# Kernel tuning notes

Hardware: AMD Instinct MI355X
Metric: run time of the kernel (lower is better)

## Reference

```python
import jax, jax.numpy as jnp
import numpy as np

D_MODEL = 192
D_INNER = 384          # expand(2) * d_model
HEADDIM = 12
NHEADS = 32            # d_inner // headdim
DSTATE = 16
NGROUPS = 1
CONV_DIM = D_INNER + 2 * NGROUPS * DSTATE          # 416
D_IN_PROJ = 2 * D_INNER + 2 * NGROUPS * DSTATE + NHEADS  # 832
LN_EPS = 1e-5


def silu(x):
    return x * jax.nn.sigmoid(x)


def depthwise_conv2d(x_nchw, w, b):
    # groups == channels depthwise conv, kernel 3, padding 1 (SAME)
    out = jax.lax.conv_general_dilated(
        x_nchw, w, window_strides=(1, 1), padding='SAME',
        feature_group_count=CONV_DIM,
        dimension_numbers=('NCHW', 'OIHW', 'NCHW'))
    return out + b[None, :, None, None]


def setup_inputs() -> dict:
    key = jax.random.key(0)
    ks = jax.random.split(key, 10)
    Bn, H, W = 4, 128, 128
    u = jax.random.normal(ks[0], (Bn, H, W, D_MODEL), jnp.float32)
    t = jax.random.normal(ks[1], (Bn, H, W, D_MODEL), jnp.float32)
    s_in = 1.0 / np.sqrt(D_MODEL)
    W_in = jax.random.normal(ks[2], (D_IN_PROJ, D_MODEL), jnp.float32) * s_in
    W_t_in = jax.random.normal(ks[3], (D_IN_PROJ, D_MODEL), jnp.float32) * s_in
    conv_w = jax.random.normal(ks[4], (CONV_DIM, 1, 3, 3), jnp.float32) * (1.0 / 3.0)
    conv_b = jnp.zeros((CONV_DIM,), jnp.float32)
    # dt_bias = inverse-softplus of dt sampled log-uniform in [dt_min, dt_max]
    dt0 = jnp.exp(jax.random.uniform(ks[5], (NHEADS,)) * (np.log(0.1) - np.log(0.001)) + np.log(0.001))
    dt_bias = dt0 + jnp.log(-jnp.expm1(-dt0))
    A_log = jnp.log(jax.random.uniform(ks[6], (NHEADS,), minval=1.0, maxval=16.0))
    D = jnp.ones((NHEADS,), jnp.float32)
    ln_gamma = jnp.ones((D_INNER,), jnp.float32)
    ln_beta = jnp.zeros((D_INNER,), jnp.float32)
    W_out = jax.random.normal(ks[7], (D_MODEL, D_INNER), jnp.float32) * (1.0 / np.sqrt(D_INNER))
    return dict(u=u, t=t, W_in=W_in, W_t_in=W_t_in, conv_w=conv_w, conv_b=conv_b,
                dt_bias=dt_bias, A_log=A_log, D=D, ln_gamma=ln_gamma, ln_beta=ln_beta,
                W_out=W_out)


def reference(u, t, W_in, W_t_in, conv_w, conv_b, dt_bias, A_log, D,
              ln_gamma, ln_beta, W_out):
    B0, H, W_, C0 = u.shape
    L = H * W_
    uu = u.reshape(B0, L, C0)
    tt = t.reshape(B0, L, C0)

    # in_proj on main branch: split into z, xBC, dt
    zxbcdt = uu @ W_in.T                                    # (B, L, 832)
    z = zxbcdt[..., :D_INNER]                               # (B, L, 384)
    xBC = zxbcdt[..., D_INNER:D_INNER + CONV_DIM]           # (B, L, 416)
    dt = zxbcdt[..., D_INNER + CONV_DIM:]                   # (B, L, 32)
    dt = jax.nn.softplus(dt + dt_bias)

    # t branch: only x1B1C1 part is ultimately used (C := C1)
    x1B1C1 = (tt @ W_t_in.T)[..., D_INNER:D_INNER + CONV_DIM]

    # depthwise 3x3 conv + silu on both branches
    xBC = xBC.reshape(B0, H, W_, CONV_DIM).transpose(0, 3, 1, 2)
    xBC = silu(depthwise_conv2d(xBC, conv_w, conv_b))
    xBC = xBC.transpose(0, 2, 3, 1).reshape(B0, L, CONV_DIM)

    x1B1C1 = x1B1C1.reshape(B0, H, W_, CONV_DIM).transpose(0, 3, 1, 2)
    x1B1C1 = silu(depthwise_conv2d(x1B1C1, conv_w, conv_b))
    x1B1C1 = x1B1C1.transpose(0, 2, 3, 1).reshape(B0, L, CONV_DIM)

    x = xBC[..., :D_INNER]                                  # V features (B, L, 384)
    Bk = xBC[..., D_INNER:D_INNER + NGROUPS * DSTATE]       # K (B, L, 16)
    Cq = x1B1C1[..., D_INNER + NGROUPS * DSTATE:]           # Q from t-branch (B, L, 16)

    A = -jnp.exp(A_log)                                     # (nheads,), negative

    # non-causal linear attention duality (ngroups == 1)
    V = x.reshape(B0, L, NHEADS, HEADDIM).transpose(0, 2, 1, 3)   # (B, h, L, d)
    dtT = dt.transpose(0, 2, 1)                                   # (B, h, L)
    dA = -(dtT[..., None] * A[None, :, None, None])               # ssd_positve_dA: positive
    V_scaled = V * dA
    KV = jnp.einsum('bln,bhld->bhnd', Bk, V_scaled)               # (B, h, 16, 12)
    y = jnp.einsum('bln,bhnd->bhld', Cq, KV) + V * D[None, :, None, None]
    y = y.transpose(0, 2, 1, 3).reshape(B0, L, D_INNER)

    # LayerNorm over d_inner
    mu = jnp.mean(y, axis=-1, keepdims=True)
    var = jnp.mean((y - mu) ** 2, axis=-1, keepdims=True)
    y = (y - mu) * jax.lax.rsqrt(var + LN_EPS) * ln_gamma + ln_beta

    y = y * z
    out = y @ W_out.T
    return out.reshape(B0, H, W_, C0)
```

## Files before the change

kernel.cpp:

```cpp
#include <hip/hip_runtime.h>
#include <hip/hip_bf16.h>
#include <math.h>


#define BN 4
#define HH 128
#define WWID 128
#define LTOK (HH*WWID)
#define NTOK (BN*LTOK)
#define DMODEL 192
#define DINNER 384
#define NH 32
#define HD 12
#define DST 16
#define CONVD 416
#define KVCHUNKS 64
#define PM 256
#define TILE_SH 12288
#define TILE_BY 24576
#define TROW ((size_t)NTOK*64)
#define YPAD 392

typedef __hip_bfloat16 bf16;
typedef unsigned int uint32;
typedef unsigned short ushort16;
typedef __attribute__((ext_vector_type(8))) short bf16x8;
typedef __attribute__((ext_vector_type(4))) float f32x4;
typedef __attribute__((ext_vector_type(16))) float f32x16;

__device__ __forceinline__ float bflo(uint32 v){ return __uint_as_float((v & 0xffffu) << 16); }
__device__ __forceinline__ float bfhi(uint32 v){ return __uint_as_float(v & 0xffff0000u); }
__device__ __forceinline__ ushort16 f2bf(float f){
    __hip_bfloat16 h = __float2bfloat16(f);
    return *reinterpret_cast<const ushort16*>(&h);
}
__device__ __forceinline__ float ldbf(const bf16* p){
    return __uint_as_float(((uint32)(*(const ushort16*)p)) << 16);
}
__device__ __forceinline__ float ldbfs(const short* p){
    return __uint_as_float(((uint32)(ushort16)(*p)) << 16);
}
__device__ __forceinline__ float softplusf(float x){
    return (x > 20.f) ? x : log1pf(expf(x));
}
__device__ __forceinline__ float siluf(float x){
    return x / (1.f + expf(-x));
}

union BFPK { short s[8]; bf16x8 v; };

__global__ __launch_bounds__(256) void k_prep(
    const float* __restrict__ Win, const float* __restrict__ Wout,
    const float* __restrict__ cw,
    bf16* __restrict__ Wsw, bf16* __restrict__ Wout_sh, float* __restrict__ wtr)
{
    const int i = blockIdx.x*256 + threadIdx.x;
    if (i < 832*DMODEL) {
        const int ch = i / DMODEL, k = i - ch*DMODEL;
        const int nt = ch >> 6, row = ch & 63;
        const int ks = k ^ ((row & 7) << 3);
        Wsw[(size_t)nt*TILE_SH + row*DMODEL + ks] = __float2bfloat16(Win[i]);
    }
    if (i < DMODEL*DINNER) {
        const int m = i / DINNER, k = i - m*DINNER;
        const int ni = m >> 4, mr = m & 15;
        const int ks = k >> 5, kq = (k >> 3) & 3, ii = k & 7;
        const int lane = kq*16 + mr;
        Wout_sh[(size_t)((ni*12 + ks)*64 + lane)*8 + ii] = __float2bfloat16(Wout[i]);
    }
    if (i < CONVD*9) { const int c = i/9, k = i - c*9; wtr[k*420 + c] = cw[i]; }
}

__global__ __launch_bounds__(512) void k_proj_mfma(
    const float* __restrict__ u, const bf16* __restrict__ Wsw,
    const float* __restrict__ dt_b, const float* __restrict__ A_log,
    bf16* __restrict__ z_bf, bf16* __restrict__ xbc_pre, float* __restrict__ dA)
{
    __shared__ __align__(16) short S[3*TILE_SH];

    const int tid = threadIdx.x;
    const int m0 = blockIdx.x * PM;
    const int ntbase = blockIdx.y * 7;
    const int ntiles = blockIdx.y ? 6 : 7;
    const int wid = tid >> 6, lane = tid & 63;
    const int fr = lane & 31;
    const int hi = lane >> 5;

    const char* gW = (const char*)Wsw;
    auto GLOAD = [&](int nt, int buf) {
        const char* src = gW + (size_t)nt*TILE_BY + wid*3072 + lane*16;
        char* dst = ((char*)S) + buf*TILE_BY + wid*3072;
        #pragma unroll
        for (int c = 0; c < 3; ++c)
            __builtin_amdgcn_global_load_lds(
                (const __attribute__((address_space(1))) void*)(src + c*1024),
                (__attribute__((address_space(3))) void*)(dst + c*1024), 16, 0, 0);
    };

    GLOAD(ntbase, 0);

    const float db = dt_b[fr];
    const float al = expf(A_log[fr]);
    bf16x8 a[12];
    {
        const float* arow = u + (size_t)(m0 + wid*32 + fr)*DMODEL;
        #pragma unroll
        for (int ks=0;ks<12;++ks) {
            const float4 a0 = *(const float4*)(arow + ks*16 + hi*8);
            const float4 a1 = *(const float4*)(arow + ks*16 + hi*8 + 4);
            BFPK pk;
            pk.s[0]=(short)f2bf(a0.x); pk.s[1]=(short)f2bf(a0.y);
            pk.s[2]=(short)f2bf(a0.z); pk.s[3]=(short)f2bf(a0.w);
            pk.s[4]=(short)f2bf(a1.x); pk.s[5]=(short)f2bf(a1.y);
            pk.s[6]=(short)f2bf(a1.z); pk.s[7]=(short)f2bf(a1.w);
            a[ks] = pk.v;
        }
    }
    asm volatile("s_waitcnt vmcnt(0)" ::: "memory");
    GLOAD(ntbase + 1, 1);
    __builtin_amdgcn_s_barrier();
    __builtin_amdgcn_sched_barrier(0);

    const int kswz = (fr & 7) << 3;

    for (int i = 0; i < ntiles; ++i) {
        const int nt = ntbase + i;
        const short* Sb = &S[(i % 3)*TILE_SH];

        f32x16 acc0, acc1;
        #pragma unroll
        for (int q=0;q<16;++q) { acc0[q]=0.f; acc1[q]=0.f; }

        #pragma unroll
        for (int ks=0;ks<12;++ks) {
            const int kk = (ks*16 + hi*8) ^ kswz;
            const bf16x8 b0 = *(const bf16x8*)&Sb[fr*DMODEL + kk];
            const bf16x8 b1 = *(const bf16x8*)&Sb[(32+fr)*DMODEL + kk];
            acc0 = __builtin_amdgcn_mfma_f32_32x32x16_bf16(a[ks], b0, acc0, 0, 0, 0);
            acc1 = __builtin_amdgcn_mfma_f32_32x32x16_bf16(a[ks], b1, acc1, 0, 0, 0);
        }

        #pragma unroll
        for (int ni=0;ni<2;++ni) {
            const f32x16& ac = ni ? acc1 : acc0;
            const int n0 = nt*64 + ni*32;
            if (n0 < DINNER) {
                bf16* dst = z_bf + (size_t)nt*TROW + (ni*32 + fr);
                #pragma unroll
                for (int r=0;r<16;++r) {
                    const int tok = m0 + wid*32 + (r&3) + 8*(r>>2) + 4*hi;
                    dst[(size_t)tok*64] = __float2bfloat16(ac[r]);
                }
            } else if (n0 < 800) {
                const int loc = n0 - DINNER + fr;
                bf16* dst = xbc_pre + (size_t)(loc>>6)*TROW + (loc & 63);
                #pragma unroll
                for (int r=0;r<16;++r) {
                    const int tok = m0 + wid*32 + (r&3) + 8*(r>>2) + 4*hi;
                    dst[(size_t)tok*64] = __float2bfloat16(ac[r]);
                }
            } else {
                #pragma unroll
                for (int r=0;r<16;++r) {
                    const int tok = m0 + wid*32 + (r&3) + 8*(r>>2) + 4*hi;
                    const float dt = softplusf(ac[r] + db);
                    dA[(size_t)tok*NH + fr] = dt * al;
                }
            }
        }

        if (i + 2 < ntiles) {
            GLOAD(nt + 2, (i + 2) % 3);
            asm volatile("s_waitcnt vmcnt(35)" ::: "memory");
        } else {
            asm volatile("s_waitcnt vmcnt(32)" ::: "memory");
        }
        __builtin_amdgcn_s_barrier();
        __builtin_amdgcn_sched_barrier(0);
    }
}

__global__ __launch_bounds__(256) void k_tproj(
    const float* __restrict__ t, const float* __restrict__ Wtin, float* __restrict__ cq_pre)
{
    __shared__ float ts[16][196];
    __shared__ float ws[16][196];
    const int tid = threadIdx.x;
    const int tok0 = blockIdx.x * 16;
    #pragma unroll
    for (int i = 0; i < 3; ++i) {
        const int flat = tid + 256*i;
        const int row = flat / 48, c = (flat % 48)*4;
        *(float4*)&ts[row][c] = *(const float4*)(t    + (size_t)(tok0+row)*DMODEL + c);
        *(float4*)&ws[row][c] = *(const float4*)(Wtin + (size_t)(784+row)*DMODEL + c);
    }
    __syncthreads();
    const int tt = tid >> 4, n = tid & 15;
    float s0=0.f,s1=0.f,s2=0.f,s3=0.f;
    #pragma unroll 4
    for (int k = 0; k < DMODEL; k += 4) {
        s0 = fmaf(ts[tt][k+0], ws[n][k+0], s0);
        s1 = fmaf(ts[tt][k+1], ws[n][k+1], s1);
        s2 = fmaf(ts[tt][k+2], ws[n][k+2], s2);
        s3 = fmaf(ts[tt][k+3], ws[n][k+3], s3);
    }
    cq_pre[(size_t)(tok0+tt)*DST + n] = (s0+s1)+(s2+s3);
}

__global__ __launch_bounds__(416) void k_conv416(
    const bf16* __restrict__ in, const float* __restrict__ wtr, const float* __restrict__ cb,
    bf16* __restrict__ out)
{
    __shared__ float ws[9*420];
    __shared__ float bs[416];
    const int tid = threadIdx.x;
    for (int i = tid; i < 9*420; i += 416) ws[i] = wtr[i];
    if (tid < 416) bs[tid] = cb[tid];
    __syncthreads();

    const int pl  = tid / 52;
    const int grp = tid - pl*52;
    const int c0  = grp*8;
    const int pix = blockIdx.x*8 + pl;
    const int hw  = pix & (LTOK-1);
    const int h = hw >> 7, w = hw & 127;
    const int bb = pix >> 14;

    const bf16* inT = in + (size_t)(c0 >> 6)*TROW + (c0 & 63);

    float acc[8];
    {
        const float4 b0 = *(const float4*)&bs[c0];
        const float4 b1 = *(const float4*)&bs[c0+4];
        acc[0]=b0.x; acc[1]=b0.y; acc[2]=b0.z; acc[3]=b0.w;
        acc[4]=b1.x; acc[5]=b1.y; acc[6]=b1.z; acc[7]=b1.w;
    }

    #pragma unroll
    for (int dh=-1; dh<=1; ++dh) {
        const int hh = h + dh;
        if ((unsigned)hh >= (unsigned)HH) continue;
        #pragma unroll
        for (int dw=-1; dw<=1; ++dw) {
            const int w2 = w + dw;
            if ((unsigned)w2 >= (unsigned)WWID) continue;
            const int wi = (dh+1)*3 + (dw+1);
            const int pix2 = (bb<<14) + (hh<<7) + w2;
            const uint4 v = *(const uint4*)((const ushort16*)inT + (size_t)pix2*64);
            const float4 w0 = *(const float4*)&ws[wi*420 + c0];
            const float4 w1 = *(const float4*)&ws[wi*420 + c0 + 4];
            acc[0] = fmaf(bflo(v.x), w0.x, acc[0]);
            acc[1] = fmaf(bfhi(v.x), w0.y, acc[1]);
            acc[2] = fmaf(bflo(v.y), w0.z, acc[2]);
            acc[3] = fmaf(bfhi(v.y), w0.w, acc[3]);
            acc[4] = fmaf(bflo(v.z), w1.x, acc[4]);
            acc[5] = fmaf(bfhi(v.z), w1.y, acc[5]);
            acc[6] = fmaf(bflo(v.w), w1.z, acc[6]);
            acc[7] = fmaf(bfhi(v.w), w1.w, acc[7]);
        }
    }

    uint4 o;
    o.x = ((uint32)f2bf(siluf(acc[1])) << 16) | (uint32)f2bf(siluf(acc[0]));
    o.y = ((uint32)f2bf(siluf(acc[3])) << 16) | (uint32)f2bf(siluf(acc[2]));
    o.z = ((uint32)f2bf(siluf(acc[5])) << 16) | (uint32)f2bf(siluf(acc[4]));
    o.w = ((uint32)f2bf(siluf(acc[7])) << 16) | (uint32)f2bf(siluf(acc[6]));
    *(uint4*)((ushort16*)out + (size_t)pix*CONVD + c0) = o;
}

__global__ __launch_bounds__(256) void k_conv16(
    const float* __restrict__ in, const float* __restrict__ cw, const float* __restrict__ cb,
    bf16* __restrict__ out)
{
    const int idx = blockIdx.x*256 + threadIdx.x;
    const int cc = idx & 15;
    const int pix = idx >> 4;
    const int hw = pix & (LTOK-1);
    const int h = hw >> 7, w = hw & 127;
    const int bb = pix >> 14;
    const int c = 400 + cc;

    float wg[9];
    #pragma unroll
    for (int k=0;k<9;++k) wg[k] = cw[c*9+k];
    float a = cb[c];
    #pragma unroll
    for (int dh=-1; dh<=1; ++dh) {
        const int hh = h + dh;
        if ((unsigned)hh >= (unsigned)HH) continue;
        #pragma unroll
        for (int dw=-1; dw<=1; ++dw) {
            const int w2 = w + dw;
            if ((unsigned)w2 >= (unsigned)WWID) continue;
            a = fmaf(in[((size_t)((bb<<14)+(hh<<7)+w2))*16 + cc], wg[(dh+1)*3 + (dw+1)], a);
        }
    }
    out[(size_t)pix*16 + cc] = __float2bfloat16(siluf(a));
}

__global__ __launch_bounds__(512) void k_kv(
    const bf16* __restrict__ xbc_post, const float* __restrict__ dA,
    float* __restrict__ partial)
{
    __shared__ short vsb[16][408];
    __shared__ float das[16][32];
    const int tid = threadIdx.x;
    const int b = blockIdx.y;
    const int n = tid & 15;
    const int g = tid >> 4;

    float acc[12];
    #pragma unroll
    for (int j=0;j<12;++j) acc[j]=0.f;

    const int l0base = b*LTOK + blockIdx.x*256;

    for (int it = 0; it < 16; ++it) {
        const int l0 = l0base + it*16;
        for (int i = tid; i < 16*200; i += 512) {
            const int tok = i / 200;
            const int c2 = i - tok*200;
            const uint32 v = *(const uint32*)((const ushort16*)xbc_post
                                + (size_t)(l0+tok)*CONVD + c2*2);
            *(uint32*)&vsb[tok][c2*2] = v;
        }
        {
            const int tok = tid >> 5, h = tid & 31;
            das[tok][h] = dA[(size_t)(l0+tok)*NH + h];
        }
        __syncthreads();

        #pragma unroll
        for (int tok = 0; tok < 16; ++tok) {
            const uint32 bkraw = (uint32)(ushort16)vsb[tok][DINNER + n];
            const float s = __uint_as_float(bkraw << 16) * das[tok][g];
            const uint32* vp = (const uint32*)&vsb[tok][g*12];
            const uint32 w0 = vp[0], w1 = vp[1], w2 = vp[2];
            acc[0]  = fmaf(s, bflo(w0), acc[0]);
            acc[1]  = fmaf(s, bfhi(w0), acc[1]);
            acc[2]  = fmaf(s, bflo(w1), acc[2]);
            acc[3]  = fmaf(s, bfhi(w1), acc[3]);
            acc[4]  = fmaf(s, bflo(w2), acc[4]);
            acc[5]  = fmaf(s, bfhi(w2), acc[5]);
            const uint32* vq = (const uint32*)&vsb[tok][g*12 + 6];
            const uint32 w3 = vq[0], w4 = vq[1], w5 = vq[2];
            acc[6]  = fmaf(s, bflo(w3), acc[6]);
            acc[7]  = fmaf(s, bfhi(w3), acc[7]);
            acc[8]  = fmaf(s, bflo(w4), acc[8]);
            acc[9]  = fmaf(s, bfhi(w4), acc[9]);
            acc[10] = fmaf(s, bflo(w5), acc[10]);
            acc[11] = fmaf(s, bfhi(w5), acc[11]);
        }
        __syncthreads();
    }

    float* dst = partial + ((size_t)(b*KVCHUNKS + blockIdx.x))*6144 + (size_t)tid*12;
    #pragma unroll
    for (int j4=0;j4<3;++j4)
        *(float4*)(dst + j4*4) = make_float4(acc[j4*4], acc[j4*4+1], acc[j4*4+2], acc[j4*4+3]);
}

__global__ __launch_bounds__(256) void k_kvred(
    const float* __restrict__ partial, bf16* __restrict__ kvhl)
{
    const int idx = blockIdx.x*256 + threadIdx.x;
    const int b = idx / 6144;
    const int rem = idx - b*6144;
    const int hd = rem >> 4, n = rem & 15;
    const int h = hd / HD, d = hd - h*HD;
    const float* p = partial + (size_t)(b*KVCHUNKS)*6144 + h*192 + n*12 + d;
    float s = 0.f;
    #pragma unroll 4
    for (int c = 0; c < KVCHUNKS; ++c) s += p[(size_t)c*6144];
    const bf16 hi = __float2bfloat16(s);
    const float hif = ldbf(&hi);
    kvhl[((size_t)b*2 + 0)*6144 + rem] = hi;
    kvhl[((size_t)b*2 + 1)*6144 + rem] = __float2bfloat16(s - hif);
}

__global__ __launch_bounds__(256) void k_ynorm_out(
    const bf16* __restrict__ xbc_post, const bf16* __restrict__ cq_bf,
    const bf16* __restrict__ z_bf, const bf16* __restrict__ kvhl,
    const float* __restrict__ Dv, const float* __restrict__ ln_g, const float* __restrict__ ln_b,
    const bf16* __restrict__ Wout_sh, float* __restrict__ out)
{
    __shared__ __align__(16) short yzs[64*YPAD];
    __shared__ float gs[DINNER], bs2[DINNER], ds[DINNER];
    const int tid = threadIdx.x;
    const int token0 = blockIdx.x * 64;
    const int b = token0 >> 14;

    {
        const int row = tid >> 2, seg = tid & 3;
        const short* src = (const short*)xbc_post + (size_t)(token0+row)*CONVD + seg*96;
        short* dst = &yzs[row*YPAD + seg*96];
        #pragma unroll
        for (int j = 0; j < 12; ++j)
            *(uint4*)(dst + j*8) = *(const uint4*)(src + j*8);
    }

    for (int i = tid; i < DINNER; i += 256) {
        gs[i]  = ln_g[i];
        bs2[i] = ln_b[i];
        ds[i]  = Dv[i/HD];
    }
    __syncthreads();

    const int wid = tid >> 6, lane = tid & 63;
    const int fr = lane & 15, fq = lane >> 4;
    const int tokA = token0 + wid*16;

    const bf16x8 cqf = *(const bf16x8*)((const short*)cq_bf + (size_t)(tokA+fr)*DST + (fq&1)*8);

    const short* kvsrc = (const short*)kvhl + ((size_t)b*2 + (fq >> 1))*6144
                         + (size_t)fr*16 + (fq & 1)*8;

    f32x4 acc[24];
    #pragma unroll
    for (int t = 0; t < 24; ++t) {
        const bf16x8 bfv = *(const bf16x8*)(kvsrc + t*256);
        f32x4 z4 = (f32x4){0.f,0.f,0.f,0.f};
        acc[t] = __builtin_amdgcn_mfma_f32_16x16x32_bf16(cqf, bfv, z4, 0, 0, 0);
    }

    const int rloc0 = wid*16 + fq*4;
    const int tokj0 = tokA + fq*4;
    float s[4]  = {0.f,0.f,0.f,0.f};
    float s2[4] = {0.f,0.f,0.f,0.f};
    #pragma unroll
    for (int t = 0; t < 24; ++t) {
        const int hd = t*16 + fr;
        const float dvh = ds[hd];
        #pragma unroll
        for (int j = 0; j < 4; ++j) {
            const float vv = ldbfs(&yzs[(rloc0+j)*YPAD + hd]);
            const float y = fmaf(vv, dvh, acc[t][j]);
            acc[t][j] = y;
            s[j] += y;
            s2[j] = fmaf(y, y, s2[j]);
        }
    }
    #pragma unroll
    for (int j = 0; j < 4; ++j) {
        #pragma unroll
        for (int off = 8; off > 0; off >>= 1) {
            s[j]  += __shfl_xor(s[j],  off, 16);
            s2[j] += __shfl_xor(s2[j], off, 16);
        }
    }
    float mu[4], rs[4];
    #pragma unroll
    for (int j = 0; j < 4; ++j) {
        mu[j] = s[j] * (1.f/384.f);
        const float var = s2[j]*(1.f/384.f) - mu[j]*mu[j];
        rs[j] = rsqrtf(var + 1e-5f);
    }

    #pragma unroll
    for (int t = 0; t < 24; ++t) {
        const int hd = t*16 + fr;
        const float g = gs[hd], be = bs2[hd];
        const bf16* zsrc = z_bf + (size_t)(hd>>6)*TROW + (hd & 63);
        #pragma unroll
        for (int j = 0; j < 4; ++j) {
            const int tok = tokj0 + j;
            const float yn = fmaf((acc[t][j] - mu[j])*rs[j], g, be);
            const float zv = ldbf(zsrc + (size_t)tok*64);
            yzs[(rloc0+j)*YPAD + hd] = (short)f2bf(yn*zv);
        }
    }

    const short* yrow = &yzs[(wid*16 + fr)*YPAD];
    bf16x8 af[12];
    #pragma unroll
    for (int ks = 0; ks < 12; ++ks)
        af[ks] = *(const bf16x8*)(yrow + ks*32 + fq*8);

    f32x4 oacc[12];
    #pragma unroll
    for (int ni = 0; ni < 12; ++ni) oacc[ni] = (f32x4){0.f,0.f,0.f,0.f};

    #pragma unroll
    for (int ks = 0; ks < 12; ++ks) {
        #pragma unroll
        for (int ni = 0; ni < 12; ++ni) {
            const bf16x8 bw = *(const bf16x8*)((const short*)Wout_sh
                                + (size_t)((ni*12 + ks)*64 + lane)*8);
            oacc[ni] = __builtin_amdgcn_mfma_f32_16x16x32_bf16(af[ks], bw, oacc[ni], 0, 0, 0);
        }
    }

    #pragma unroll
    for (int ni = 0; ni < 12; ++ni) {
        const int n = ni*16 + fr;
        #pragma unroll
        for (int r = 0; r < 4; ++r)
            out[(size_t)(tokj0 + r)*DMODEL + n] = oacc[ni][r];
    }
}

extern "C" void kernel_launch(void* const* d_in, const int* in_sizes, int n_in,
                              void* d_out, int out_size, void* d_ws, size_t ws_size,
                              hipStream_t stream)
{
    const float* u      = (const float*)d_in[0];
    const float* t      = (const float*)d_in[1];
    const float* Win    = (const float*)d_in[2];
    const float* Wtin   = (const float*)d_in[3];
    const float* conv_w = (const float*)d_in[4];
    const float* conv_b = (const float*)d_in[5];
    const float* dt_b   = (const float*)d_in[6];
    const float* A_log  = (const float*)d_in[7];
    const float* Dv     = (const float*)d_in[8];
    const float* ln_g   = (const float*)d_in[9];
    const float* ln_bt  = (const float*)d_in[10];
    const float* W_out  = (const float*)d_in[11];
    float* out = (float*)d_out;

    char* p = (char*)d_ws;
    bf16* z_bf     = (bf16*)p;  p += (size_t)6*TROW*2;
    bf16* xbc_pre  = (bf16*)p;  p += (size_t)7*TROW*2;
    bf16* xbc_post = (bf16*)p;  p += (size_t)NTOK*CONVD*2;
    float* cq_pre  = (float*)p; p += (size_t)NTOK*DST*4;
    bf16* cq_bf    = (bf16*)p;  p += (size_t)NTOK*DST*2;
    float* dA      = (float*)p; p += (size_t)NTOK*NH*4;
    bf16* kvhl     = (bf16*)p;  p += (size_t)BN*2*6144*2;
    bf16* Wsw      = (bf16*)p;  p += (size_t)832*DMODEL*2;
    bf16* Wout_sh  = (bf16*)p;  p += (size_t)DMODEL*DINNER*2;
    float* wtr     = (float*)p; p += (size_t)9*420*4;

    float* kv_part = (float*)xbc_pre;

    k_prep<<<624, 256, 0, stream>>>(Win, W_out, conv_w, Wsw, Wout_sh, wtr);
    k_proj_mfma<<<dim3(NTOK/PM, 2), 512, 0, stream>>>(u, Wsw, dt_b, A_log, z_bf, xbc_pre, dA);
    k_tproj<<<NTOK/16, 256, 0, stream>>>(t, Wtin, cq_pre);
    k_conv416<<<NTOK/8, 416, 0, stream>>>(xbc_pre, wtr, conv_b, xbc_post);
    k_conv16<<<NTOK*16/256, 256, 0, stream>>>(cq_pre, conv_w, conv_b, cq_bf);
    k_kv<<<dim3(KVCHUNKS, BN), 512, 0, stream>>>(xbc_post, dA, kv_part);
    k_kvred<<<BN*6144/256, 256, 0, stream>>>(kv_part, kvhl);
    k_ynorm_out<<<NTOK/64, 256, 0, stream>>>(xbc_post, cq_bf, z_bf, kvhl,
                                             Dv, ln_g, ln_bt, Wout_sh, out);
}
```

Measured before the change: 291.7 us.

## Register-tile depthwise conv to 2x4 outputs per thread for input reuse

Each thread in the 416-channel depthwise conv now computes a 2-row by 4-column patch of output pixels instead of one. Each input pixel loaded from global memory is reused across every output that needs it, so one thread reads 4x6 pixels rather than 9 per output. The grid shrinks eightfold, and each block covers 2 rows by 32 columns. In exchange, register use rises (64 accumulators per thread), and fewer blocks may limit occupancy and latency hiding.

```diff
diff --git a/kernel.cpp b/kernel.cpp
--- a/kernel.cpp
+++ b/kernel.cpp
@@ -221,51 +221,78 @@
     const int pl  = tid / 52;
     const int grp = tid - pl*52;
     const int c0  = grp*8;
-    const int pix = blockIdx.x*8 + pl;
-    const int hw  = pix & (LTOK-1);
-    const int h = hw >> 7, w = hw & 127;
-    const int bb = pix >> 14;
+    const int bid = blockIdx.x;
+    const int bb  = bid >> 8;
+    const int rem = bid & 255;
+    const int h0  = (rem >> 2) << 1;
+    const int w0  = ((rem & 3) << 5) + pl*4;
 
     const bf16* inT = in + (size_t)(c0 >> 6)*TROW + (c0 & 63);
 
-    float acc[8];
+    float acc[2][4][8];
     {
         const float4 b0 = *(const float4*)&bs[c0];
         const float4 b1 = *(const float4*)&bs[c0+4];
-        acc[0]=b0.x; acc[1]=b0.y; acc[2]=b0.z; acc[3]=b0.w;
-        acc[4]=b1.x; acc[5]=b1.y; acc[6]=b1.z; acc[7]=b1.w;
-    }
-
-    #pragma unroll
-    for (int dh=-1; dh<=1; ++dh) {
-        const int hh = h + dh;
-        if ((unsigned)hh >= (unsigned)HH) continue;
-        #pragma unroll
-        for (int dw=-1; dw<=1; ++dw) {
-            const int w2 = w + dw;
-            if ((unsigned)w2 >= (unsigned)WWID) continue;
-            const int wi = (dh+1)*3 + (dw+1);
-            const int pix2 = (bb<<14) + (hh<<7) + w2;
-            const uint4 v = *(const uint4*)((const ushort16*)inT + (size_t)pix2*64);
-            const float4 w0 = *(const float4*)&ws[wi*420 + c0];
-            const float4 w1 = *(const float4*)&ws[wi*420 + c0 + 4];
-            acc[0] = fmaf(bflo(v.x), w0.x, acc[0]);
-            acc[1] = fmaf(bfhi(v.x), w0.y, acc[1]);
-            acc[2] = fmaf(bflo(v.y), w0.z, acc[2]);
-            acc[3] = fmaf(bfhi(v.y), w0.w, acc[3]);
-            acc[4] = fmaf(bflo(v.z), w1.x, acc[4]);
-            acc[5] = fmaf(bfhi(v.z), w1.y, acc[5]);
-            acc[6] = fmaf(bflo(v.w), w1.z, acc[6]);
-            acc[7] = fmaf(bfhi(v.w), w1.w, acc[7]);
-        }
-    }
-
-    uint4 o;
-    o.x = ((uint32)f2bf(siluf(acc[1])) << 16) | (uint32)f2bf(siluf(acc[0]));
-    o.y = ((uint32)f2bf(siluf(acc[3])) << 16) | (uint32)f2bf(siluf(acc[2]));
-    o.z = ((uint32)f2bf(siluf(acc[5])) << 16) | (uint32)f2bf(siluf(acc[4]));
-    o.w = ((uint32)f2bf(siluf(acc[7])) << 16) | (uint32)f2bf(siluf(acc[6]));
-    *(uint4*)((ushort16*)out + (size_t)pix*CONVD + c0) = o;
+        #pragma unroll
+        for (int v2 = 0; v2 < 2; ++v2)
+            #pragma unroll
+            for (int u = 0; u < 4; ++u) {
+                acc[v2][u][0]=b0.x; acc[v2][u][1]=b0.y;
+                acc[v2][u][2]=b0.z; acc[v2][u][3]=b0.w;
+                acc[v2][u][4]=b1.x; acc[v2][u][5]=b1.y;
+                acc[v2][u][6]=b1.z; acc[v2][u][7]=b1.w;
+            }
+    }
+
+    #pragma unroll
+    for (int dr=-1; dr<=2; ++dr) {
+        const int rr = h0 + dr;
+        if ((unsigned)rr >= (unsigned)HH) continue;
+        const int rowb = (bb<<14) + (rr<<7);
+        #pragma unroll
+        for (int dc=-1; dc<=4; ++dc) {
+            const int wc = w0 + dc;
+            if ((unsigned)wc >= (unsigned)WWID) continue;
+            const uint4 v = *(const uint4*)((const ushort16*)inT + (size_t)(rowb + wc)*64);
+            const float x0=bflo(v.x), x1=bfhi(v.x), x2=bflo(v.y), x3=bfhi(v.y);
+            const float x4=bflo(v.z), x5=bfhi(v.z), x6=bflo(v.w), x7=bfhi(v.w);
+            #pragma unroll
+            for (int v2 = 0; v2 < 2; ++v2) {
+                const int dh = dr - v2;
+                if (dh < -1 || dh > 1) continue;
+                #pragma unroll
+                for (int u = 0; u < 4; ++u) {
+                    const int dw = dc - u;
+                    if (dw < -1 || dw > 1) continue;
+                    const int wi = (dh+1)*3 + (dw+1);
+                    const float4 w0v = *(const float4*)&ws[wi*420 + c0];
+                    const float4 w1v = *(const float4*)&ws[wi*420 + c0 + 4];
+                    acc[v2][u][0]=fmaf(x0,w0v.x,acc[v2][u][0]);
+                    acc[v2][u][1]=fmaf(x1,w0v.y,acc[v2][u][1]);
+                    acc[v2][u][2]=fmaf(x2,w0v.z,acc[v2][u][2]);
+                    acc[v2][u][3]=fmaf(x3,w0v.w,acc[v2][u][3]);
+                    acc[v2][u][4]=fmaf(x4,w1v.x,acc[v2][u][4]);
+                    acc[v2][u][5]=fmaf(x5,w1v.y,acc[v2][u][5]);
+                    acc[v2][u][6]=fmaf(x6,w1v.z,acc[v2][u][6]);
+                    acc[v2][u][7]=fmaf(x7,w1v.w,acc[v2][u][7]);
+                }
+            }
+        }
+    }
+
+    const int pix00 = (bb<<14) + (h0<<7) + w0;
+    #pragma unroll
+    for (int v2 = 0; v2 < 2; ++v2) {
+        #pragma unroll
+        for (int u = 0; u < 4; ++u) {
+            uint4 o;
+            o.x = ((uint32)f2bf(siluf(acc[v2][u][1])) << 16) | (uint32)f2bf(siluf(acc[v2][u][0]));
+            o.y = ((uint32)f2bf(siluf(acc[v2][u][3])) << 16) | (uint32)f2bf(siluf(acc[v2][u][2]));
+            o.z = ((uint32)f2bf(siluf(acc[v2][u][5])) << 16) | (uint32)f2bf(siluf(acc[v2][u][4]));
+            o.w = ((uint32)f2bf(siluf(acc[v2][u][7])) << 16) | (uint32)f2bf(siluf(acc[v2][u][6]));
+            *(uint4*)((ushort16*)out + (size_t)(pix00 + v2*WWID + u)*CONVD + c0) = o;
+        }
+    }
 }
 
 __global__ __launch_bounds__(256) void k_conv16(
@@ -534,7 +561,7 @@
     k_prep<<<624, 256, 0, stream>>>(Win, W_out, conv_w, Wsw, Wout_sh, wtr);
     k_proj_mfma<<<dim3(NTOK/PM, 2), 512, 0, stream>>>(u, Wsw, dt_b, A_log, z_bf, xbc_pre, dA);
     k_tproj<<<NTOK/16, 256, 0, stream>>>(t, Wtin, cq_pre);
-    k_conv416<<<NTOK/8, 416, 0, stream>>>(xbc_pre, wtr, conv_b, xbc_post);
+    k_conv416<<<NTOK/64, 416, 0, stream>>>(xbc_pre, wtr, conv_b, xbc_post);
     k_conv16<<<NTOK*16/256, 256, 0, stream>>>(cq_pre, conv_w, conv_b, cq_bf);
     k_kv<<<dim3(KVCHUNKS, BN), 512, 0, stream>>>(xbc_post, dA, kv_part);
     k_kvred<<<BN*6144/256, 256, 0, stream>>>(kv_part, kvhl);
```

Result: faster. 285.8 us (-2.0%).
